# Kernel optimization log

Measured on AMD Instinct MI355X. Metric: run time of the kernel, lower is better.

## Reference

```python
import jax, jax.numpy as jnp
import numpy as np

N_NODES = 100000
N_EDGES = 1600000
F_IN = 8
PERIODS = 18
UNITS = 256     # A3TGCN out_channels (unit_num)
HIDDEN = 256    # MLP hidden_units


def setup_inputs() -> dict:
    key = jax.random.key(0)
    ks = jax.random.split(key, 24)
    g = lambda k, shape, s: (jax.random.normal(k, shape, dtype=jnp.float32) * s)
    inp = {
        "x": g(ks[0], (N_NODES, F_IN, PERIODS), 1.0),
        "edge_index": jax.random.randint(ks[1], (2, N_EDGES), 0, N_NODES, dtype=jnp.int64),
        "edge_weight": jax.random.uniform(ks[2], (N_EDGES,), dtype=jnp.float32),
        # TGCN gate params: GCNConv weight/bias + Linear(2*UNITS, UNITS)
        "Wz": g(ks[3], (F_IN, UNITS), 0.1), "bz": jnp.zeros((UNITS,), jnp.float32),
        "Wlz": g(ks[4], (2 * UNITS, UNITS), 0.05), "blz": jnp.zeros((UNITS,), jnp.float32),
        "Wr": g(ks[5], (F_IN, UNITS), 0.1), "br": jnp.zeros((UNITS,), jnp.float32),
        "Wlr": g(ks[6], (2 * UNITS, UNITS), 0.05), "blr": jnp.zeros((UNITS,), jnp.float32),
        "Wh": g(ks[7], (F_IN, UNITS), 0.1), "bh": jnp.zeros((UNITS,), jnp.float32),
        "Wlh": g(ks[8], (2 * UNITS, UNITS), 0.05), "blh": jnp.zeros((UNITS,), jnp.float32),
        # temporal attention logits
        "att": jax.random.uniform(ks[9], (PERIODS,), dtype=jnp.float32),
        # MLP head
        "W1": g(ks[10], (UNITS, HIDDEN), 0.05), "b1": jnp.zeros((HIDDEN,), jnp.float32),
        "W2": g(ks[11], (HIDDEN, HIDDEN), 0.05), "b2": jnp.zeros((HIDDEN,), jnp.float32),
        "W3": g(ks[12], (HIDDEN, HIDDEN), 0.05), "b3": jnp.zeros((HIDDEN,), jnp.float32),
        "Wo": g(ks[13], (HIDDEN, PERIODS), 0.05), "bo": jnp.zeros((PERIODS,), jnp.float32),
    }
    return inp


def _gcn_norm(edge_index, edge_weight, n_nodes):
    # PyG gcn_norm with add_self_loops=True, improved=False
    src, dst = edge_index[0], edge_index[1]
    loop = jnp.arange(n_nodes, dtype=src.dtype)
    src_a = jnp.concatenate([src, loop])
    dst_a = jnp.concatenate([dst, loop])
    w_a = jnp.concatenate([edge_weight, jnp.ones((n_nodes,), edge_weight.dtype)])
    deg = jax.ops.segment_sum(w_a, dst_a, num_segments=n_nodes)
    dinv = jnp.where(deg > 0, jax.lax.rsqrt(jnp.where(deg > 0, deg, 1.0)), 0.0)
    norm = dinv[src_a] * w_a * dinv[dst_a]
    return src_a, dst_a, norm


def reference(x, edge_index, edge_weight, Wz, bz, Wlz, blz, Wr, br, Wlr, blr,
              Wh, bh, Wlh, blh, att, W1, b1, W2, b2, W3, b3, Wo, bo):
    n_nodes = x.shape[0]
    src, dst, norm = _gcn_norm(edge_index, edge_weight, n_nodes)

    def gconv(X, W, b):
        m = (X @ W)[src] * norm[:, None]                       # [E+N, UNITS]
        return jax.ops.segment_sum(m, dst, num_segments=n_nodes) + b

    probs = jax.nn.softmax(att)

    def step(carry, inp):
        H, acc = carry
        Xt, p = inp                                            # Xt: [N, F_IN]
        Z = jax.nn.sigmoid(jnp.concatenate([gconv(Xt, Wz, bz), H], 1) @ Wlz + blz)
        R = jax.nn.sigmoid(jnp.concatenate([gconv(Xt, Wr, br), H], 1) @ Wlr + blr)
        Ht = jnp.tanh(jnp.concatenate([gconv(Xt, Wh, bh), H * R], 1) @ Wlh + blh)
        H = Z * H + (1.0 - Z) * Ht
        return (H, acc + p * H), None

    xs = jnp.transpose(x, (2, 0, 1))                           # [T, N, F_IN]
    init = (jnp.zeros((n_nodes, UNITS), x.dtype), jnp.zeros((n_nodes, UNITS), x.dtype))
    (_, h), _ = jax.lax.scan(step, init, (xs, probs))

    h = jax.nn.relu(h)
    h = jax.nn.relu(h @ W1 + b1)
    h = jax.nn.relu(h @ W2 + b2)
    h = jax.nn.relu(h @ W3 + b3)
    return h @ Wo + bo                                         # [N, PERIODS]
```

## Files before the change

### kernel.cpp

```cpp
#include <hip/hip_runtime.h>

typedef _Float16 h8 __attribute__((ext_vector_type(8)));
typedef _Float16 h2 __attribute__((ext_vector_type(2)));
typedef float f4 __attribute__((ext_vector_type(4)));

#define N_NODES 100000
#define NPAD    100096
#define N_EDGES 1600000
#define T_P  18
#define U    256
#define KP   288
#define LDW  296
#define NB_SCAN 391

#define LOG2E  1.44269504f
#define LOG2E2 2.88539008f

__global__ void k_init_deg(float* deg){
    int i = blockIdx.x*256 + threadIdx.x;
    if (i < N_NODES) deg[i] = 1.0f;
}
__global__ void k_deg(const int* __restrict__ ei, const float* __restrict__ w, float* deg){
    int e = blockIdx.x*256 + threadIdx.x;
    if (e < N_EDGES) atomicAdd(&deg[ei[N_EDGES + e]], w[e]);
}
__global__ void k_dinv(const float* deg, float* dinv){
    int i = blockIdx.x*256 + threadIdx.x;
    if (i < N_NODES) dinv[i] = rsqrtf(deg[i]);
}
__global__ void k_count(const int* __restrict__ ei, int* cnt){
    int e = blockIdx.x*256 + threadIdx.x;
    if (e < N_EDGES) atomicAdd(&cnt[ei[N_EDGES + e]], 1);
}
__global__ void k_partial(const int* __restrict__ cnt, int* part){
    __shared__ int red[256];
    int b = blockIdx.x, i = b*256 + threadIdx.x;
    red[threadIdx.x] = (i < N_NODES) ? cnt[i] : 0;
    __syncthreads();
    for (int d = 128; d > 0; d >>= 1){
        if (threadIdx.x < d) red[threadIdx.x] += red[threadIdx.x + d];
        __syncthreads();
    }
    if (threadIdx.x == 0) part[b] = red[0];
}
__global__ void k_scan_part(const int* __restrict__ part, int* pbase){
    __shared__ int s[512];
    int tid = threadIdx.x;
    int v = (tid < NB_SCAN) ? part[tid] : 0;
    s[tid] = v; __syncthreads();
    for (int d = 1; d < 512; d <<= 1){
        int t2 = (tid >= d) ? s[tid - d] : 0;
        __syncthreads();
        s[tid] += t2;
        __syncthreads();
    }
    if (tid < NB_SCAN) pbase[tid] = s[tid] - v;
}
__global__ void k_emit(const int* __restrict__ cnt, const int* __restrict__ pbase,
                       int* rowp, int* ccur){
    __shared__ int s[256];
    int b = blockIdx.x, tid = threadIdx.x, i = b*256 + tid;
    int v = (i < N_NODES) ? cnt[i] : 0;
    s[tid] = v; __syncthreads();
    for (int d = 1; d < 256; d <<= 1){
        int t2 = (tid >= d) ? s[tid - d] : 0;
        __syncthreads();
        s[tid] += t2;
        __syncthreads();
    }
    int excl = s[tid] - v + pbase[b];
    if (i < N_NODES){
        rowp[i] = excl; ccur[i] = excl;
        if (i == N_NODES - 1) rowp[N_NODES] = excl + v;
    }
}
__global__ void k_scatter(const int* __restrict__ ei, const float* __restrict__ w,
                          const float* __restrict__ dinv, int* ccur,
                          int* __restrict__ csrc, float* __restrict__ cnrm){
    int e = blockIdx.x*256 + threadIdx.x;
    if (e >= N_EDGES) return;
    int s = ei[e], d = ei[N_EDGES + e];
    int pos = atomicAdd(&ccur[d], 1);
    csrc[pos] = s;
    cnrm[pos] = dinv[s] * w[e] * dinv[d];
}
__global__ void k_gather_nf(const float* __restrict__ x, const float* __restrict__ dinv,
                            const int* __restrict__ rowp, const int* __restrict__ csrc,
                            const float* __restrict__ cnrm, _Float16* __restrict__ AXh){
    int idx = blockIdx.x*256 + threadIdx.x;
    if (idx >= N_NODES*8) return;
    int n = idx >> 3, f = idx & 7;
    float dv = dinv[n];
    float w0 = dv * dv;
    const float* xb = x + (size_t)n*144 + f*18;
    float s[T_P];
    #pragma unroll
    for (int t = 0; t < T_P; t++) s[t] = w0 * xb[t];
    int p1 = rowp[n+1];
    for (int p = rowp[n]; p < p1; p++){
        float w = cnrm[p];
        const float* xs = x + (size_t)csrc[p]*144 + f*18;
        #pragma unroll
        for (int t = 0; t < T_P; t++) s[t] += w * xs[t];
    }
    #pragma unroll
    for (int t = 0; t < T_P; t++)
        AXh[((size_t)t*NPAD + n)*8 + f] = (_Float16)s[t];
}

__global__ void k_probs(const float* att, float* probs){
    if (threadIdx.x == 0 && blockIdx.x == 0){
        float mx = -1e30f;
        for (int t = 0; t < T_P; t++) mx = fmaxf(mx, att[t]);
        float e[T_P], s = 0.f;
        for (int t = 0; t < T_P; t++){ e[t] = __expf(att[t] - mx); s += e[t]; }
        for (int t = 0; t < T_P; t++) probs[t] = e[t] / s;
    }
}
__global__ void k_wprime(const float* Wz, const float* bz, const float* Wlz, const float* blz,
                         const float* Wr, const float* br, const float* Wlr, const float* blr,
                         const float* Wh, const float* bh, const float* Wlh, const float* blh,
                         float* wprime, float* biasg){
    int idx = blockIdx.x*256 + threadIdx.x;
    if (idx >= 3*9*256) return;
    int g = idx / (9*256); int rem = idx - g*9*256;
    int row = rem / 256;   int u = rem - row*256;
    const float* W  = g==0 ? Wz  : (g==1 ? Wr  : Wh);
    const float* Wl = g==0 ? Wlz : (g==1 ? Wlr : Wlh);
    const float* bb = g==0 ? bz  : (g==1 ? br  : bh);
    const float* bl = g==0 ? blz : (g==1 ? blr : blh);
    float s = 0.f;
    if (row < 8){
        for (int c = 0; c < U; c++) s += W[row*U + c] * Wl[c*U + u];
        wprime[(g*8 + row)*U + u] = s;
    } else {
        for (int c = 0; c < U; c++) s += bb[c] * Wl[c*U + u];
        biasg[g*U + u] = s + bl[u];
    }
}
__global__ void k_fill_gates(const float* __restrict__ wprime, const float* __restrict__ Wlz,
                             const float* __restrict__ Wlr, const float* __restrict__ Wlh,
                             _Float16* __restrict__ B1t, _Float16* __restrict__ B2t){
    int idx = blockIdx.x*256 + threadIdx.x;
    if (idx >= 768*KP) return;
    int n = idx / KP, k = idx - n*KP;
    int g = (n < 256) ? 0 : ((n < 512) ? 1 : 2);
    int u = n & 255;
    const float* Wl = g==0 ? Wlz : (g==1 ? Wlr : Wlh);
    float v;
    if (k < 8)        v = wprime[(g*8 + k)*U + u];
    else if (k < 264) v = Wl[(256 + (k - 8))*U + u];
    else              v = 0.f;
    if (n < 512) B1t[(size_t)n*KP + k] = (_Float16)v;
    else         B2t[(size_t)(n - 512)*KP + k] = (_Float16)v;
}
__global__ void k_fill_mlp(const float* __restrict__ W1, const float* __restrict__ W2,
                           const float* __restrict__ W3, const float* __restrict__ Wo,
                           _Float16* W1t, _Float16* W2t, _Float16* W3t, _Float16* WoT){
    int idx = blockIdx.x*256 + threadIdx.x;
    if (idx >= 3*U*KP + 64*KP) return;
    if (idx < 3*U*KP){
        int l = idx / (U*KP); int rem = idx - l*U*KP;
        int n = rem / KP, k = rem - n*KP;
        const float* W = l==0 ? W1 : (l==1 ? W2 : W3);
        _Float16*   Wt = l==0 ? W1t : (l==1 ? W2t : W3t);
        Wt[(size_t)n*KP + k] = (k >= 8 && k < 264) ? (_Float16)W[(size_t)(k-8)*U + n] : (_Float16)0.f;
    } else {
        int rem = idx - 3*U*KP;
        int n = rem / KP, k = rem - n*KP;
        WoT[(size_t)n*KP + k] = (n < T_P && k >= 8 && k < 264) ? (_Float16)Wo[(size_t)(k-8)*T_P + n] : (_Float16)0.f;
    }
}

__device__ __forceinline__ void gemm_pass(const _Float16* sbuf, const _Float16* __restrict__ Bg,
                                          int brow, int lr, int lq, f4* g){
    for (int kt = 0; kt < 9; kt++){
        h8 af[4], bf[2];
        #pragma unroll
        for (int i = 0; i < 4; i++)
            af[i] = *(const h8*)(sbuf + (i*16 + lr)*LDW + kt*32 + lq*8);
        #pragma unroll
        for (int j = 0; j < 2; j++)
            bf[j] = *(const h8*)(Bg + (size_t)(brow + j*16 + lr)*KP + kt*32 + lq*8);
        #pragma unroll
        for (int i = 0; i < 4; i++)
            #pragma unroll
            for (int j = 0; j < 2; j++)
                g[i*2 + j] = __builtin_amdgcn_mfma_f32_16x16x32_f16(af[i], bf[j], g[i*2 + j], 0, 0, 0);
    }
}
__device__ __forceinline__ void gemm_pass2(const _Float16* sbuf, const _Float16* __restrict__ Bg,
                                           int browZ, int browR, int lr, int lq, f4* gz, f4* gr){
    for (int kt = 0; kt < 9; kt++){
        h8 af[4], bz_[2], br_[2];
        #pragma unroll
        for (int i = 0; i < 4; i++)
            af[i] = *(const h8*)(sbuf + (i*16 + lr)*LDW + kt*32 + lq*8);
        #pragma unroll
        for (int j = 0; j < 2; j++){
            bz_[j] = *(const h8*)(Bg + (size_t)(browZ + j*16 + lr)*KP + kt*32 + lq*8);
            br_[j] = *(const h8*)(Bg + (size_t)(browR + j*16 + lr)*KP + kt*32 + lq*8);
        }
        #pragma unroll
        for (int i = 0; i < 4; i++)
            #pragma unroll
            for (int j = 0; j < 2; j++){
                gz[i*2 + j] = __builtin_amdgcn_mfma_f32_16x16x32_f16(af[i], bz_[j], gz[i*2 + j], 0, 0, 0);
                gr[i*2 + j] = __builtin_amdgcn_mfma_f32_16x16x32_f16(af[i], br_[j], gr[i*2 + j], 0, 0, 0);
            }
    }
}

__global__ __attribute__((amdgpu_waves_per_eu(2, 2))) __launch_bounds__(512)
void k_fused(const _Float16* __restrict__ AXh,
             const _Float16* __restrict__ B1t, const _Float16* __restrict__ B2t,
             const float* __restrict__ biasg,
             const _Float16* __restrict__ W1t, const _Float16* __restrict__ W2t,
             const _Float16* __restrict__ W3t, const _Float16* __restrict__ WoT,
             const float* __restrict__ b1, const float* __restrict__ b2,
             const float* __restrict__ b3, const float* __restrict__ bo,
             const float* __restrict__ probs, float* __restrict__ dout){
    __shared__ __align__(16) _Float16 sA[64*LDW];
    __shared__ __align__(16) _Float16 sB[64*LDW];
    const int tid  = threadIdx.x;
    const int wave = tid >> 6, lane = tid & 63;
    const int lr = lane & 15, lq = lane >> 4;
    const int wc = wave * 32;
    const int n0 = blockIdx.x * 64;

    {
        uint* w0 = (uint*)sA; uint* w1 = (uint*)sB;
        for (int i = tid; i < 64*LDW/2; i += 512){ w0[i] = 0u; w1[i] = 0u; }
    }
    __syncthreads();
    if (tid < 64)
        *(uint4*)(&sA[tid*LDW]) = *(const uint4*)(AXh + ((size_t)0*NPAD + n0 + tid)*8);

    float bz_r[2], br_r[2], bh_r[2];
    #pragma unroll
    for (int j = 0; j < 2; j++){
        int col = wc + j*16 + lr;
        bz_r[j] = -LOG2E  * biasg[col];
        br_r[j] = -LOG2E  * biasg[256 + col];
        bh_r[j] =  LOG2E2 * biasg[512 + col];
    }

    h2 acc[16], hr[16];
    h2 z2 = {(_Float16)0.f, (_Float16)0.f};
    #pragma unroll
    for (int k = 0; k < 16; k++){ acc[k] = z2; hr[k] = z2; }

    const f4 fz = {0.f, 0.f, 0.f, 0.f};
    __syncthreads();

    for (int t = 0; t < T_P; t++){
        const float pt = probs[t];
        const int last = (t == T_P - 1);
        uint4 ld;
        if (tid < 64){
            if (!last) ld = *(const uint4*)(AXh + ((size_t)(t+1)*NPAD + n0 + tid)*8);
        } else if (tid < 128){
            ld = *(const uint4*)(AXh + ((size_t)t*NPAD + n0 + (tid-64))*8);
        }
        f4 gz[8], gr[8];
        #pragma unroll
        for (int k = 0; k < 8; k++){ gz[k] = fz; gr[k] = fz; }
        gemm_pass2(sA, B1t, wc, 256 + wc, lr, lq, gz, gr);
        #pragma unroll
        for (int i = 0; i < 4; i++)
            #pragma unroll
            for (int j = 0; j < 2; j++)
                #pragma unroll
                for (int r = 0; r < 4; r++){
                    int v = (i*2 + j)*4 + r;
                    int row = i*16 + lq*4 + r;
                    int col = wc + j*16 + lr;
                    float rr = __builtin_amdgcn_rcpf(
                        1.f + __builtin_amdgcn_exp2f(fmaf(gr[i*2 + j][r], -LOG2E, br_r[j])));
                    sB[row*LDW + 8 + col] = (_Float16)((float)hr[v>>1][v&1] * rr);
                }
        if (tid >= 64 && tid < 128)
            *(uint4*)(&sB[(tid-64)*LDW]) = ld;
        __syncthreads();
        f4 g[8];
        #pragma unroll
        for (int k = 0; k < 8; k++) g[k] = fz;
        gemm_pass(sB, B2t, wc, lr, lq, g);
        #pragma unroll
        for (int i = 0; i < 4; i++)
            #pragma unroll
            for (int j = 0; j < 2; j++)
                #pragma unroll
                for (int r = 0; r < 4; r++){
                    int v = (i*2 + j)*4 + r;
                    int row = i*16 + lq*4 + r;
                    int col = wc + j*16 + lr;
                    float e2 = __builtin_amdgcn_exp2f(fmaf(g[i*2 + j][r], LOG2E2, bh_r[j]));
                    float ht = fmaf(-2.f, __builtin_amdgcn_rcpf(e2 + 1.f), 1.f);
                    float z  = __builtin_amdgcn_rcpf(
                        1.f + __builtin_amdgcn_exp2f(fmaf(gz[i*2 + j][r], -LOG2E, bz_r[j])));
                    float h  = (float)hr[v>>1][v&1];
                    float hn = fmaf(z, h - ht, ht);
                    float a  = fmaf(pt, hn, (float)acc[v>>1][v&1]);
                    acc[v>>1][v&1] = (_Float16)a;
                    hr[v>>1][v&1]  = (_Float16)hn;
                    sA[row*LDW + 8 + col] = (_Float16)(last ? fmaxf(a, 0.f) : hn);
                }
        if (!last && tid < 64)
            *(uint4*)(&sA[tid*LDW]) = ld;
        __syncthreads();
    }

    #pragma unroll
    for (int l = 0; l < 3; l++){
        const _Float16* Wt = (l == 0) ? W1t : (l == 1) ? W2t : W3t;
        const float*    bl = (l == 0) ? b1  : (l == 1) ? b2  : b3;
        float blv[2];
        #pragma unroll
        for (int j = 0; j < 2; j++) blv[j] = bl[wc + j*16 + lr];
        f4 g[8];
        #pragma unroll
        for (int k = 0; k < 8; k++) g[k] = fz;
        gemm_pass(sA, Wt, wc, lr, lq, g);
        __syncthreads();
        #pragma unroll
        for (int i = 0; i < 4; i++)
            #pragma unroll
            for (int j = 0; j < 2; j++)
                #pragma unroll
                for (int r = 0; r < 4; r++){
                    int row = i*16 + lq*4 + r;
                    int col = wc + j*16 + lr;
                    sA[row*LDW + 8 + col] = (_Float16)fmaxf(g[i*2 + j][r] + blv[j], 0.f);
                }
        __syncthreads();
    }
    if (wave == 0){
        f4 g[8];
        #pragma unroll
        for (int k = 0; k < 8; k++) g[k] = fz;
        gemm_pass(sA, WoT, 0, lr, lq, g);
        #pragma unroll
        for (int i = 0; i < 4; i++)
            #pragma unroll
            for (int j = 0; j < 2; j++)
                #pragma unroll
                for (int r = 0; r < 4; r++){
                    int row = i*16 + lq*4 + r;
                    int col = j*16 + lr;
                    int gm = n0 + row;
                    if (col < T_P && gm < N_NODES)
                        dout[(size_t)gm*T_P + col] = g[i*2 + j][r] + bo[col];
                }
    }
}

extern "C" void kernel_launch(void* const* d_in, const int* in_sizes, int n_in,
                              void* d_out, int out_size, void* d_ws, size_t ws_size,
                              hipStream_t stream){
    const float* x   = (const float*)d_in[0];
    const int*   ei  = (const int*)  d_in[1];
    const float* ew  = (const float*)d_in[2];
    const float* Wz  = (const float*)d_in[3];  const float* bz  = (const float*)d_in[4];
    const float* Wlz = (const float*)d_in[5];  const float* blz = (const float*)d_in[6];
    const float* Wr  = (const float*)d_in[7];  const float* br  = (const float*)d_in[8];
    const float* Wlr = (const float*)d_in[9];  const float* blr = (const float*)d_in[10];
    const float* Wh  = (const float*)d_in[11]; const float* bh  = (const float*)d_in[12];
    const float* Wlh = (const float*)d_in[13]; const float* blh = (const float*)d_in[14];
    const float* att = (const float*)d_in[15];
    const float* W1  = (const float*)d_in[16]; const float* b1  = (const float*)d_in[17];
    const float* W2  = (const float*)d_in[18]; const float* b2  = (const float*)d_in[19];
    const float* W3  = (const float*)d_in[20]; const float* b3  = (const float*)d_in[21];
    const float* Wo  = (const float*)d_in[22]; const float* bo  = (const float*)d_in[23];
    float* dout = (float*)d_out;

    char* ws = (char*)d_ws; size_t off = 0;
    auto alloc = [&](size_t bytes)->char*{ char* p = ws + off; off += (bytes + 255) & ~(size_t)255; return p; };
    _Float16* AXh   = (_Float16*)alloc((size_t)T_P*NPAD*8*2);
    float*    deg   = (float*)alloc((size_t)N_NODES*4);
    float*    dinv  = (float*)alloc((size_t)N_NODES*4);
    int*      cnt   = (int*)  alloc((size_t)N_NODES*4);
    int*      rowp  = (int*)  alloc(((size_t)N_NODES + 1)*4);
    int*      ccur  = (int*)  alloc((size_t)N_NODES*4);
    int*      csrc  = (int*)  alloc((size_t)N_EDGES*4);
    float*    cnrm  = (float*)alloc((size_t)N_EDGES*4);
    int*      part  = (int*)  alloc((size_t)NB_SCAN*4);
    int*      pbase = (int*)  alloc((size_t)NB_SCAN*4);
    float*    wprime= (float*)alloc((size_t)3*8*U*4);
    float*    biasg = (float*)alloc((size_t)3*U*4);
    _Float16* B1t   = (_Float16*)alloc((size_t)512*KP*2);
    _Float16* B2t   = (_Float16*)alloc((size_t)256*KP*2);
    _Float16* W1t   = (_Float16*)alloc((size_t)U*KP*2);
    _Float16* W2t   = (_Float16*)alloc((size_t)U*KP*2);
    _Float16* W3t   = (_Float16*)alloc((size_t)U*KP*2);
    _Float16* WoT   = (_Float16*)alloc((size_t)64*KP*2);
    float*    probs = (float*)alloc((size_t)T_P*4);

    hipMemsetAsync(AXh, 0, (size_t)T_P*NPAD*8*2, stream);
    hipMemsetAsync(cnt, 0, (size_t)N_NODES*4, stream);

    k_probs<<<1, 64, 0, stream>>>(att, probs);
    k_wprime<<<(3*9*256 + 255)/256, 256, 0, stream>>>(Wz,bz,Wlz,blz, Wr,br,Wlr,blr, Wh,bh,Wlh,blh, wprime, biasg);
    k_fill_gates<<<(768*KP + 255)/256, 256, 0, stream>>>(wprime, Wlz, Wlr, Wlh, B1t, B2t);
    k_fill_mlp<<<(3*U*KP + 64*KP + 255)/256, 256, 0, stream>>>(W1, W2, W3, Wo, W1t, W2t, W3t, WoT);

    k_init_deg<<<(N_NODES + 255)/256, 256, 0, stream>>>(deg);
    k_deg<<<(N_EDGES + 255)/256, 256, 0, stream>>>(ei, ew, deg);
    k_dinv<<<(N_NODES + 255)/256, 256, 0, stream>>>(deg, dinv);
    k_count<<<(N_EDGES + 255)/256, 256, 0, stream>>>(ei, cnt);
    k_partial<<<NB_SCAN, 256, 0, stream>>>(cnt, part);
    k_scan_part<<<1, 512, 0, stream>>>(part, pbase);
    k_emit<<<NB_SCAN, 256, 0, stream>>>(cnt, pbase, rowp, ccur);
    k_scatter<<<(N_EDGES + 255)/256, 256, 0, stream>>>(ei, ew, dinv, ccur, csrc, cnrm);
    k_gather_nf<<<(N_NODES*8 + 255)/256, 256, 0, stream>>>(x, dinv, rowp, csrc, cnrm, AXh);

    k_fused<<<NPAD/64, 512, 0, stream>>>(AXh, B1t, B2t, biasg, W1t, W2t, W3t, WoT,
                                         b1, b2, b3, bo, probs, dout);
}
```

Measured before the change: 2.420 ms.

## Process two 64-row tiles per block with ping-pong buffers to overlap stages

Each block now handles 128 nodes as two 64-row tiles (X and Y) and interleaves their gate GEMMs, epilogues and shared-memory writes. One tile's epilogue and writes can then run between the other tile's GEMMs, and weight fetches from global memory are shared across twice as many rows. The MLP head is interleaved across both tiles in the same way. In exchange register pressure roughly doubles for the hidden and accumulator state at a fixed two waves per EU, which risks spills, and the grid is halved to 782 blocks.

```diff
diff --git a/kernel.cpp b/kernel.cpp
--- a/kernel.cpp
+++ b/kernel.cpp
@@ -211,6 +211,101 @@
     }
 }
 
+__device__ __forceinline__ void epi_zr(const f4 (&gz)[8], const f4 (&gr)[8],
+                                       const h2 (&hr)[16], h2 (&z)[16], h2 (&hrr)[16],
+                                       const float (&bzr)[2], const float (&brr)[2]){
+    #pragma unroll
+    for (int i = 0; i < 4; i++)
+        #pragma unroll
+        for (int j = 0; j < 2; j++)
+            #pragma unroll
+            for (int r = 0; r < 4; r++){
+                int v = (i*2 + j)*4 + r;
+                float zf = __builtin_amdgcn_rcpf(
+                    1.f + __builtin_amdgcn_exp2f(fmaf(gz[i*2 + j][r], -LOG2E, bzr[j])));
+                float rf = __builtin_amdgcn_rcpf(
+                    1.f + __builtin_amdgcn_exp2f(fmaf(gr[i*2 + j][r], -LOG2E, brr[j])));
+                z[v>>1][v&1]   = (_Float16)zf;
+                hrr[v>>1][v&1] = (_Float16)((float)hr[v>>1][v&1] * rf);
+            }
+}
+__device__ __forceinline__ void epi_upd(const f4 (&g)[8], const h2 (&z)[16],
+                                        h2 (&hr)[16], h2 (&acc)[16],
+                                        const float (&bhr)[2], float pt){
+    #pragma unroll
+    for (int i = 0; i < 4; i++)
+        #pragma unroll
+        for (int j = 0; j < 2; j++)
+            #pragma unroll
+            for (int r = 0; r < 4; r++){
+                int v = (i*2 + j)*4 + r;
+                float e2 = __builtin_amdgcn_exp2f(fmaf(g[i*2 + j][r], LOG2E2, bhr[j]));
+                float ht = fmaf(-2.f, __builtin_amdgcn_rcpf(e2 + 1.f), 1.f);
+                float zf = (float)z[v>>1][v&1];
+                float h  = (float)hr[v>>1][v&1];
+                float hn = fmaf(zf, h - ht, ht);
+                acc[v>>1][v&1] = (_Float16)fmaf(pt, hn, (float)acc[v>>1][v&1]);
+                hr[v>>1][v&1]  = (_Float16)hn;
+            }
+}
+__device__ __forceinline__ void write_h16(_Float16* s, const h2 (&val)[16],
+                                          int lq, int lr, int wc){
+    #pragma unroll
+    for (int i = 0; i < 4; i++)
+        #pragma unroll
+        for (int j = 0; j < 2; j++)
+            #pragma unroll
+            for (int r = 0; r < 4; r++){
+                int v = (i*2 + j)*4 + r;
+                s[(i*16 + lq*4 + r)*LDW + 8 + wc + j*16 + lr] = val[v>>1][v&1];
+            }
+}
+__device__ __forceinline__ void write_relu16(_Float16* s, const h2 (&a)[16],
+                                             int lq, int lr, int wc){
+    #pragma unroll
+    for (int i = 0; i < 4; i++)
+        #pragma unroll
+        for (int j = 0; j < 2; j++)
+            #pragma unroll
+            for (int r = 0; r < 4; r++){
+                int v = (i*2 + j)*4 + r;
+                s[(i*16 + lq*4 + r)*LDW + 8 + wc + j*16 + lr] =
+                    (_Float16)fmaxf((float)a[v>>1][v&1], 0.f);
+            }
+}
+__device__ __forceinline__ void write_relu_g(_Float16* s, const f4 (&g)[8],
+                                             const float (&blv)[2], int lq, int lr, int wc){
+    #pragma unroll
+    for (int i = 0; i < 4; i++)
+        #pragma unroll
+        for (int j = 0; j < 2; j++)
+            #pragma unroll
+            for (int r = 0; r < 4; r++)
+                s[(i*16 + lq*4 + r)*LDW + 8 + wc + j*16 + lr] =
+                    (_Float16)fmaxf(g[i*2 + j][r] + blv[j], 0.f);
+}
+__device__ __forceinline__ void head_out(const _Float16* s, const _Float16* __restrict__ WoT,
+                                         const float* __restrict__ bo, float* __restrict__ dout,
+                                         int rowbase, int lr, int lq){
+    const f4 fz = {0.f, 0.f, 0.f, 0.f};
+    f4 g[8];
+    #pragma unroll
+    for (int k = 0; k < 8; k++) g[k] = fz;
+    gemm_pass(s, WoT, 0, lr, lq, g);
+    #pragma unroll
+    for (int i = 0; i < 4; i++)
+        #pragma unroll
+        for (int j = 0; j < 2; j++)
+            #pragma unroll
+            for (int r = 0; r < 4; r++){
+                int row = i*16 + lq*4 + r;
+                int col = j*16 + lr;
+                int gm = rowbase + row;
+                if (col < T_P && gm < N_NODES)
+                    dout[(size_t)gm*T_P + col] = g[i*2 + j][r] + bo[col];
+            }
+}
+
 __global__ __attribute__((amdgpu_waves_per_eu(2, 2))) __launch_bounds__(512)
 void k_fused(const _Float16* __restrict__ AXh,
              const _Float16* __restrict__ B1t, const _Float16* __restrict__ B2t,
@@ -220,21 +315,24 @@
              const float* __restrict__ b1, const float* __restrict__ b2,
              const float* __restrict__ b3, const float* __restrict__ bo,
              const float* __restrict__ probs, float* __restrict__ dout){
-    __shared__ __align__(16) _Float16 sA[64*LDW];
-    __shared__ __align__(16) _Float16 sB[64*LDW];
+    __shared__ __align__(16) _Float16 sX[64*LDW];
+    __shared__ __align__(16) _Float16 sY[64*LDW];
     const int tid  = threadIdx.x;
     const int wave = tid >> 6, lane = tid & 63;
     const int lr = lane & 15, lq = lane >> 4;
     const int wc = wave * 32;
-    const int n0 = blockIdx.x * 64;
+    const int n0 = blockIdx.x * 128;
 
     {
-        uint* w0 = (uint*)sA; uint* w1 = (uint*)sB;
+        uint* w0 = (uint*)sX; uint* w1 = (uint*)sY;
         for (int i = tid; i < 64*LDW/2; i += 512){ w0[i] = 0u; w1[i] = 0u; }
     }
     __syncthreads();
     if (tid < 64)
-        *(uint4*)(&sA[tid*LDW]) = *(const uint4*)(AXh + ((size_t)0*NPAD + n0 + tid)*8);
+        *(uint4*)(&sX[tid*LDW]) = *(const uint4*)(AXh + ((size_t)0*NPAD + n0 + tid)*8);
+    uint4 ldY;
+    if (tid >= 64 && tid < 128)
+        ldY = *(const uint4*)(AXh + ((size_t)0*NPAD + n0 + tid)*8);
 
     float bz_r[2], br_r[2], bh_r[2];
     #pragma unroll
@@ -245,10 +343,12 @@
         bh_r[j] =  LOG2E2 * biasg[512 + col];
     }
 
-    h2 acc[16], hr[16];
+    h2 accX[16], hrX[16], accY[16], hrY[16], zX[16], zY[16], hrrX[16], hrrY[16];
     h2 z2 = {(_Float16)0.f, (_Float16)0.f};
     #pragma unroll
-    for (int k = 0; k < 16; k++){ acc[k] = z2; hr[k] = z2; }
+    for (int k = 0; k < 16; k++){
+        accX[k] = z2; hrX[k] = z2; accY[k] = z2; hrY[k] = z2;
+    }
 
     const f4 fz = {0.f, 0.f, 0.f, 0.f};
     __syncthreads();
@@ -256,61 +356,56 @@
     for (int t = 0; t < T_P; t++){
         const float pt = probs[t];
         const int last = (t == T_P - 1);
-        uint4 ld;
-        if (tid < 64){
-            if (!last) ld = *(const uint4*)(AXh + ((size_t)(t+1)*NPAD + n0 + tid)*8);
-        } else if (tid < 128){
-            ld = *(const uint4*)(AXh + ((size_t)t*NPAD + n0 + (tid-64))*8);
+        uint4 ldX;
+        if (tid < 64 && !last)
+            ldX = *(const uint4*)(AXh + ((size_t)(t+1)*NPAD + n0 + tid)*8);
+
+        f4 gz[8], gr[8];
+        #pragma unroll
+        for (int k = 0; k < 8; k++){ gz[k] = fz; gr[k] = fz; }
+        gemm_pass2(sX, B1t, wc, 256 + wc, lr, lq, gz, gr);
+        epi_zr(gz, gr, hrX, zX, hrrX, bz_r, br_r);
+        write_h16(sY, hrY, lq, lr, wc);
+        if (tid >= 64 && tid < 128){
+            *(uint4*)(&sY[(tid-64)*LDW]) = ldY;
+            if (!last)
+                ldY = *(const uint4*)(AXh + ((size_t)(t+1)*NPAD + n0 + tid)*8);
         }
-        f4 gz[8], gr[8];
+        __syncthreads();
+
+        write_h16(sX, hrrX, lq, lr, wc);
         #pragma unroll
         for (int k = 0; k < 8; k++){ gz[k] = fz; gr[k] = fz; }
-        gemm_pass2(sA, B1t, wc, 256 + wc, lr, lq, gz, gr);
-        #pragma unroll
-        for (int i = 0; i < 4; i++)
-            #pragma unroll
-            for (int j = 0; j < 2; j++)
-                #pragma unroll
-                for (int r = 0; r < 4; r++){
-                    int v = (i*2 + j)*4 + r;
-                    int row = i*16 + lq*4 + r;
-                    int col = wc + j*16 + lr;
-                    float rr = __builtin_amdgcn_rcpf(
-                        1.f + __builtin_amdgcn_exp2f(fmaf(gr[i*2 + j][r], -LOG2E, br_r[j])));
-                    sB[row*LDW + 8 + col] = (_Float16)((float)hr[v>>1][v&1] * rr);
-                }
-        if (tid >= 64 && tid < 128)
-            *(uint4*)(&sB[(tid-64)*LDW]) = ld;
-        __syncthreads();
-        f4 g[8];
-        #pragma unroll
-        for (int k = 0; k < 8; k++) g[k] = fz;
-        gemm_pass(sB, B2t, wc, lr, lq, g);
-        #pragma unroll
-        for (int i = 0; i < 4; i++)
-            #pragma unroll
-            for (int j = 0; j < 2; j++)
-                #pragma unroll
-                for (int r = 0; r < 4; r++){
-                    int v = (i*2 + j)*4 + r;
-                    int row = i*16 + lq*4 + r;
-                    int col = wc + j*16 + lr;
-                    float e2 = __builtin_amdgcn_exp2f(fmaf(g[i*2 + j][r], LOG2E2, bh_r[j]));
-                    float ht = fmaf(-2.f, __builtin_amdgcn_rcpf(e2 + 1.f), 1.f);
-                    float z  = __builtin_amdgcn_rcpf(
-                        1.f + __builtin_amdgcn_exp2f(fmaf(gz[i*2 + j][r], -LOG2E, bz_r[j])));
-                    float h  = (float)hr[v>>1][v&1];
-                    float hn = fmaf(z, h - ht, ht);
-                    float a  = fmaf(pt, hn, (float)acc[v>>1][v&1]);
-                    acc[v>>1][v&1] = (_Float16)a;
-                    hr[v>>1][v&1]  = (_Float16)hn;
-                    sA[row*LDW + 8 + col] = (_Float16)(last ? fmaxf(a, 0.f) : hn);
-                }
+        gemm_pass2(sY, B1t, wc, 256 + wc, lr, lq, gz, gr);
+        epi_zr(gz, gr, hrY, zY, hrrY, bz_r, br_r);
+        __syncthreads();
+
+        {
+            f4 g[8];
+            #pragma unroll
+            for (int k = 0; k < 8; k++) g[k] = fz;
+            gemm_pass(sX, B2t, wc, lr, lq, g);
+            epi_upd(g, zX, hrX, accX, bh_r, pt);
+        }
+        write_h16(sY, hrrY, lq, lr, wc);
+        __syncthreads();
+
+        if (last) write_relu16(sX, accX, lq, lr, wc);
+        else      write_h16(sX, hrX, lq, lr, wc);
         if (!last && tid < 64)
-            *(uint4*)(&sA[tid*LDW]) = ld;
-        __syncthreads();
-    }
-
+            *(uint4*)(&sX[tid*LDW]) = ldX;
+        {
+            f4 g[8];
+            #pragma unroll
+            for (int k = 0; k < 8; k++) g[k] = fz;
+            gemm_pass(sY, B2t, wc, lr, lq, g);
+            epi_upd(g, zY, hrY, accY, bh_r, pt);
+        }
+        __syncthreads();
+    }
+
+    f4 gX[8], gY[8];
+    float blvP[2] = {0.f, 0.f};
     #pragma unroll
     for (int l = 0; l < 3; l++){
         const _Float16* Wt = (l == 0) ? W1t : (l == 1) ? W2t : W3t;
@@ -318,41 +413,23 @@
         float blv[2];
         #pragma unroll
         for (int j = 0; j < 2; j++) blv[j] = bl[wc + j*16 + lr];
-        f4 g[8];
-        #pragma unroll
-        for (int k = 0; k < 8; k++) g[k] = fz;
-        gemm_pass(sA, Wt, wc, lr, lq, g);
-        __syncthreads();
-        #pragma unroll
-        for (int i = 0; i < 4; i++)
-            #pragma unroll
-            for (int j = 0; j < 2; j++)
-                #pragma unroll
-                for (int r = 0; r < 4; r++){
-                    int row = i*16 + lq*4 + r;
-                    int col = wc + j*16 + lr;
-                    sA[row*LDW + 8 + col] = (_Float16)fmaxf(g[i*2 + j][r] + blv[j], 0.f);
-                }
-        __syncthreads();
-    }
-    if (wave == 0){
-        f4 g[8];
-        #pragma unroll
-        for (int k = 0; k < 8; k++) g[k] = fz;
-        gemm_pass(sA, WoT, 0, lr, lq, g);
-        #pragma unroll
-        for (int i = 0; i < 4; i++)
-            #pragma unroll
-            for (int j = 0; j < 2; j++)
-                #pragma unroll
-                for (int r = 0; r < 4; r++){
-                    int row = i*16 + lq*4 + r;
-                    int col = j*16 + lr;
-                    int gm = n0 + row;
-                    if (col < T_P && gm < N_NODES)
-                        dout[(size_t)gm*T_P + col] = g[i*2 + j][r] + bo[col];
-                }
-    }
+        #pragma unroll
+        for (int k = 0; k < 8; k++) gX[k] = fz;
+        gemm_pass(sX, Wt, wc, lr, lq, gX);
+        if (l == 0) write_relu16(sY, accY, lq, lr, wc);
+        else        write_relu_g(sY, gY, blvP, lq, lr, wc);
+        __syncthreads();
+        write_relu_g(sX, gX, blv, lq, lr, wc);
+        #pragma unroll
+        for (int k = 0; k < 8; k++) gY[k] = fz;
+        gemm_pass(sY, Wt, wc, lr, lq, gY);
+        __syncthreads();
+        blvP[0] = blv[0]; blvP[1] = blv[1];
+    }
+    write_relu_g(sY, gY, blvP, lq, lr, wc);
+    __syncthreads();
+    if (wave == 0)      head_out(sX, WoT, bo, dout, n0,      lr, lq);
+    else if (wave == 1) head_out(sY, WoT, bo, dout, n0 + 64, lr, lq);
 }
 
 extern "C" void kernel_launch(void* const* d_in, const int* in_sizes, int n_in,
@@ -414,6 +491,6 @@
     k_scatter<<<(N_EDGES + 255)/256, 256, 0, stream>>>(ei, ew, dinv, ccur, csrc, cnrm);
     k_gather_nf<<<(N_NODES*8 + 255)/256, 256, 0, stream>>>(x, dinv, rowp, csrc, cnrm, AXh);
 
-    k_fused<<<NPAD/64, 512, 0, stream>>>(AXh, B1t, B2t, biasg, W1t, W2t, W3t, WoT,
-                                         b1, b2, b3, bo, probs, dout);
-}
+    k_fused<<<NPAD/128, 512, 0, stream>>>(AXh, B1t, B2t, biasg, W1t, W2t, W3t, WoT,
+                                          b1, b2, b3, bo, probs, dout);
+}
```

After: 3.015 ms. 24.6% more time.
